# Kernel optimization log

Measured on AMD Instinct MI355X. Metric: run time of the kernel, lower is better.

## Reference

```python
import jax, jax.numpy as jnp
import numpy as np

B, S, D, H = 2, 2048, 1024, 16
DK = D // H
NEG = -1e9


def setup_inputs() -> dict:
    key = jax.random.key(0)
    ks = jax.random.split(key, 12)
    inp = {
        "query": jax.random.normal(ks[0], (B, S, D), jnp.float32),
        "key": jax.random.normal(ks[1], (B, S, D), jnp.float32),
        "value": jax.random.normal(ks[2], (B, S, D), jnp.float32),
        "mask": jax.random.randint(ks[3], (B, S), 0, 2, jnp.int32),
    }
    # 4 linears (q, k, v, out), each d_model x d_model with bias.
    scale = 1.0 / np.sqrt(D)
    for i, name in enumerate(["wq", "wk", "wv", "wo"]):
        inp[name] = jax.random.uniform(ks[4 + i], (D, D), jnp.float32, -scale, scale)
        inp["b" + name[1]] = jax.random.uniform(ks[8 + i], (D,), jnp.float32, -scale, scale)
    return inp


def _split_heads(x):  # [B,S,D] -> [B,H,S,DK]
    return x.reshape(B, S, H, DK).transpose(0, 2, 1, 3)


def reference(query, key, value, mask, wq, bq, wk, bk, wv, bv, wo, bo):
    q = _split_heads(query @ wq.T + bq)
    k = _split_heads(key @ wk.T + bk)
    v = _split_heads(value @ wv.T + bv)
    scores = jnp.einsum("bhqd,bhkd->bhqk", q, k) / jnp.sqrt(jnp.float32(DK))
    # mask: [B,S] -> [B,1,1,S]; masked_fill where mask == 0
    m = mask[:, None, None, :]
    scores = jnp.where(m == 0, NEG, scores)
    attn = jax.nn.softmax(scores, axis=-1)  # dropout p=0 (eval) -> identity
    x = jnp.einsum("bhqk,bhkd->bhqd", attn, v)
    x = x.transpose(0, 2, 1, 3).reshape(B, S, D)
    return x @ wo.T + bo
```

## Files before the change

### kernel.cpp

```cpp
#include <hip/hip_runtime.h>


typedef _Float16 f16;
typedef _Float16 f16x8 __attribute__((ext_vector_type(8)));
typedef _Float16 f16x4 __attribute__((ext_vector_type(4)));
typedef __fp16 fp16x2r __attribute__((ext_vector_type(2)));
typedef float f32x4 __attribute__((ext_vector_type(4)));

union F16x4u { f16x4 v; fp16x2r h[2]; };

#define MFMA_F16(a, b, c) __builtin_amdgcn_mfma_f32_16x16x32_f16((a), (b), (c), 0, 0, 0)
#define MFMA16(a, b, c) __builtin_amdgcn_mfma_f32_16x16x16f16((a), (b), (c), 0, 0, 0)
#define L2E 1.44269504088896340736f

__device__ __forceinline__ void gld16(const void* g, void* l) {
    __builtin_amdgcn_global_load_lds(
        (__attribute__((address_space(1))) void*)(g),
        (__attribute__((address_space(3))) void*)(l), 16, 0, 0);
}

__global__ __launch_bounds__(256) void cvt_kernel(
    const float* __restrict__ q, const float* __restrict__ k,
    const float* __restrict__ v,
    const float* __restrict__ wq, const float* __restrict__ wk,
    const float* __restrict__ wv, const float* __restrict__ wo,
    f16* __restrict__ oq, f16* __restrict__ ok, f16* __restrict__ ov,
    f16* __restrict__ owq, f16* __restrict__ owk, f16* __restrict__ owv,
    f16* __restrict__ owo)
{
    const int z = blockIdx.y;
    const float* src;
    f16* dst;
    int n;
    switch (z) {
        case 0: src = q;  dst = oq;  n = 4194304; break;
        case 1: src = k;  dst = ok;  n = 4194304; break;
        case 2: src = v;  dst = ov;  n = 4194304; break;
        case 3: src = wq; dst = owq; n = 1048576; break;
        case 4: src = wk; dst = owk; n = 1048576; break;
        case 5: src = wv; dst = owv; n = 1048576; break;
        default: src = wo; dst = owo; n = 1048576; break;
    }
    int idx = (blockIdx.x * 256 + threadIdx.x) * 8;
    if (idx >= n) return;
    float4 a = *(const float4*)(src + idx);
    float4 b = *(const float4*)(src + idx + 4);
    f16x8 h = { (f16)a.x, (f16)a.y, (f16)a.z, (f16)a.w,
                (f16)b.x, (f16)b.y, (f16)b.z, (f16)b.w };
    *(f16x8*)(dst + idx) = h;
}

__global__ __launch_bounds__(256) void proj_qkv_kernel(
    const f16* __restrict__ xq, const f16* __restrict__ xk,
    const f16* __restrict__ xv,
    const f16* __restrict__ wqh, const f16* __restrict__ wkh,
    const f16* __restrict__ wvh,
    const float* __restrict__ bq, const float* __restrict__ bk,
    const float* __restrict__ bv,
    f16* __restrict__ qh, f16* __restrict__ kh, f16* __restrict__ vt)
{
    const int z = blockIdx.z;
    const f16* X = (z == 0) ? xq : (z == 1) ? xk : xv;
    const f16* W = (z == 0) ? wqh : (z == 1) ? wkh : wvh;
    const float* bias = (z == 0) ? bq : (z == 1) ? bk : bv;
    const f16* P0 = (z < 2) ? W : X;
    const f16* P1 = (z < 2) ? X : W;

    __shared__ __align__(16) f16 smem[16384];
    f16* As = smem;
    f16* Bs = smem + 8192;
    f16* L  = smem;

    const int t = threadIdx.x;
    const int wave = t >> 6, lane = t & 63, quad = lane >> 4, l15 = lane & 15;
    const int m_base = (wave >> 1) * 64, n_base = (wave & 1) * 64;
    const int blockM = (z < 2) ? blockIdx.y * 128 : blockIdx.x * 128;
    const int blockN = (z < 2) ? blockIdx.x * 128 : blockIdx.y * 128;

    const int srow = lane >> 3;
    const int sblk = (lane & 7) ^ srow;

    f32x4 acc[4][4];
#pragma unroll
    for (int mt = 0; mt < 4; mt++)
#pragma unroll
        for (int nt = 0; nt < 4; nt++)
            acc[mt][nt] = (f32x4){0.f, 0.f, 0.f, 0.f};

    for (int k0 = 0; k0 < 1024; k0 += 64) {
        __syncthreads();
#pragma unroll
        for (int j = 0; j < 4; j++) {
            int r0 = wave * 32 + j * 8;
            gld16(&P0[(size_t)(blockM + r0 + srow) * 1024 + k0 + sblk * 8],
                  &As[r0 * 64]);
            gld16(&P1[(size_t)(blockN + r0 + srow) * 1024 + k0 + sblk * 8],
                  &Bs[r0 * 64]);
        }
        __syncthreads();

#pragma unroll
        for (int c = 0; c < 2; c++) {
            f16x8 af[4], bf[4];
#pragma unroll
            for (int mt = 0; mt < 4; mt++)
                af[mt] = *(const f16x8*)(&As[(m_base + mt * 16 + l15) * 64 +
                                             (((c * 4 + quad) ^ (l15 & 7)) << 3)]);
#pragma unroll
            for (int nt = 0; nt < 4; nt++)
                bf[nt] = *(const f16x8*)(&Bs[(n_base + nt * 16 + l15) * 64 +
                                             (((c * 4 + quad) ^ (l15 & 7)) << 3)]);
#pragma unroll
            for (int mt = 0; mt < 4; mt++)
#pragma unroll
                for (int nt = 0; nt < 4; nt++)
                    acc[mt][nt] = MFMA_F16(af[mt], bf[nt], acc[mt][nt]);
        }
    }

    if (z < 2) {
        f16* o = (z == 0) ? qh : kh;
        const float scale = (z == 0) ? 0.125f * L2E : 1.0f;
        float4 b4[4];
#pragma unroll
        for (int mt = 0; mt < 4; mt++)
            b4[mt] = *(const float4*)(&bias[blockM + m_base + mt * 16 + quad * 4]);

#pragma unroll
        for (int half = 0; half < 2; half++) {
            __syncthreads();
            if ((wave & 1) == half) {
#pragma unroll
                for (int mt = 0; mt < 4; mt++)
#pragma unroll
                    for (int nt = 0; nt < 4; nt++) {
                        f16x4 pk = {
                            (f16)((acc[mt][nt][0] + b4[mt].x) * scale),
                            (f16)((acc[mt][nt][1] + b4[mt].y) * scale),
                            (f16)((acc[mt][nt][2] + b4[mt].z) * scale),
                            (f16)((acc[mt][nt][3] + b4[mt].w) * scale) };
                        *(f16x4*)(&L[(nt * 16 + l15) * 136 +
                                     m_base + mt * 16 + quad * 4]) = pk;
                    }
            }
            __syncthreads();
#pragma unroll
            for (int pass = 0; pass < 4; pass++) {
                int unit = pass * 32 + (t >> 3);
                int hh = unit >> 6, s_loc = unit & 63;
                f16x8 vv = *(const f16x8*)(&L[s_loc * 136 + hh * 64 + (t & 7) * 8]);
                int s_glob = blockN + half * 64 + s_loc;
                int b = s_glob >> 11, s = s_glob & 2047;
                int h_glob = (blockM >> 6) + hh;
                *(f16x8*)(&o[(((size_t)(b * 16 + h_glob) * 2048 + s) << 6) +
                             (t & 7) * 8]) = vv;
            }
        }
    } else {
        float bv_[4];
#pragma unroll
        for (int nt = 0; nt < 4; nt++)
            bv_[nt] = bias[blockN + n_base + nt * 16 + l15];

#pragma unroll
        for (int half = 0; half < 2; half++) {
            __syncthreads();
            if ((wave & 1) == half) {
#pragma unroll
                for (int mt = 0; mt < 4; mt++)
#pragma unroll
                    for (int nt = 0; nt < 4; nt++) {
                        f16x4 pk = { (f16)(acc[mt][nt][0] + bv_[nt]),
                                     (f16)(acc[mt][nt][1] + bv_[nt]),
                                     (f16)(acc[mt][nt][2] + bv_[nt]),
                                     (f16)(acc[mt][nt][3] + bv_[nt]) };
                        *(f16x4*)(&L[(nt * 16 + l15) * 136 +
                                     m_base + mt * 16 + quad * 4]) = pk;
                    }
            }
            __syncthreads();
#pragma unroll
            for (int pass = 0; pass < 4; pass++) {
                int f_loc = pass * 16 + (t >> 4);
                f16x8 vv = *(const f16x8*)(&L[f_loc * 136 + (t & 15) * 8]);
                int feat = blockN + half * 64 + f_loc;
                int hh = feat >> 6, dk = feat & 63;
                int b = blockM >> 11;
                int s0 = (blockM & 2047) + (t & 15) * 8;
                *(f16x8*)(&vt[((size_t)((b * 16 + hh) * 64 + dk) << 11) + s0]) = vv;
            }
        }
    }
}

__device__ __forceinline__ void flash_stage(
    const f16* kbase, const f16* vbase, int key0,
    f16* Kb, f16* Vb, int wave, int srow8, int sblk)
{
#pragma unroll
    for (int p = 0; p < 2; p++) {
        int r0 = p * 32 + wave * 8;
        int row = r0 + srow8;
        gld16(&kbase[(size_t)(key0 + row) * 64 + sblk * 8], &Kb[r0 * 64]);
        gld16(&vbase[(size_t)row * 2048 + key0 + sblk * 8], &Vb[r0 * 64]);
    }
}

__device__ __forceinline__ void flash_phase(
    const f16* Kbuf, const f16* Vbuf, const float* bias_all, int key0,
    const f16x8 (&qf)[2][2], int quad, int l15,
    f32x4 (&O)[2][4], f32x4 (&lacc)[2])
{
    f32x4 sc[2][4];
#pragma unroll
    for (int nt = 0; nt < 4; nt++) {
        const f16* krow = &Kbuf[(nt * 16 + l15) * 64];
        f16x8 kf0 = *(const f16x8*)(&krow[(quad ^ (l15 & 7)) << 3]);
        f16x8 kf1 = *(const f16x8*)(&krow[((quad + 4) ^ (l15 & 7)) << 3]);
        float4 b4 = *(const float4*)(&bias_all[key0 + nt * 16 + quad * 4]);
#pragma unroll
        for (int cb = 0; cb < 2; cb++) {
            f32x4 z4 = (f32x4){b4.x, b4.y, b4.z, b4.w};
            z4 = MFMA_F16(kf0, qf[cb][0], z4);
            sc[cb][nt] = MFMA_F16(kf1, qf[cb][1], z4);
        }
    }
    const f16x4 ones = {(f16)1.f, (f16)1.f, (f16)1.f, (f16)1.f};
    f16x4 pf[2][4];
#pragma unroll
    for (int cb = 0; cb < 2; cb++)
#pragma unroll
        for (int nt = 0; nt < 4; nt++) {
            float p0 = exp2f(sc[cb][nt][0]);
            float p1 = exp2f(sc[cb][nt][1]);
            float p2 = exp2f(sc[cb][nt][2]);
            float p3 = exp2f(sc[cb][nt][3]);
            F16x4u u;
            u.h[0] = __builtin_amdgcn_cvt_pkrtz(p0, p1);
            u.h[1] = __builtin_amdgcn_cvt_pkrtz(p2, p3);
            pf[cb][nt] = u.v;
            lacc[cb] = MFMA16(ones, pf[cb][nt], lacc[cb]);
        }
#pragma unroll
    for (int nto = 0; nto < 4; nto++) {
        const f16* vrow = &Vbuf[(nto * 16 + l15) * 64];
#pragma unroll
        for (int nt = 0; nt < 4; nt++) {
            f16x4 vf = *(const f16x4*)(&vrow[
                (((nt * 2 + (quad >> 1)) ^ (l15 & 7)) << 3) + (quad & 1) * 4]);
            O[0][nto] = MFMA16(vf, pf[0][nt], O[0][nto]);
            O[1][nto] = MFMA16(vf, pf[1][nt], O[1][nto]);
        }
    }
}

__global__ __launch_bounds__(256) void flash_kernel(
    const f16* __restrict__ qh, const f16* __restrict__ kh,
    const f16* __restrict__ vt, const int* __restrict__ mask,
    f16* __restrict__ ctx)
{
    __shared__ __align__(16) f16 Ks0[64 * 64];
    __shared__ __align__(16) f16 Ks1[64 * 64];
    __shared__ __align__(16) f16 Vts0[64 * 64];
    __shared__ __align__(16) f16 Vts1[64 * 64];
    __shared__ float bias_all[2048];

    const int t = threadIdx.x;
    const int wave = t >> 6, lane = t & 63, quad = lane >> 4, l15 = lane & 15;
    const int bh = blockIdx.x;
    const int b = bh >> 4, h = bh & 15;
    const int q0 = blockIdx.y * 128;

    const f16* qbase = qh + (size_t)bh * (2048 * 64);
    const f16* kbase = kh + (size_t)bh * (2048 * 64);
    const f16* vbase = vt + (size_t)bh * (64 * 2048);

#pragma unroll
    for (int j = 0; j < 8; j++) {
        int i = j * 256 + t;
        bias_all[i] = (mask[b * 2048 + i] == 0) ? -1.0e9f : 0.0f;
    }

    f16x8 qf[2][2];
#pragma unroll
    for (int cb = 0; cb < 2; cb++) {
        int qrow = q0 + wave * 32 + cb * 16 + l15;
        qf[cb][0] = *(const f16x8*)(&qbase[qrow * 64 + quad * 8]);
        qf[cb][1] = *(const f16x8*)(&qbase[qrow * 64 + 32 + quad * 8]);
    }

    f32x4 O[2][4];
#pragma unroll
    for (int cb = 0; cb < 2; cb++)
#pragma unroll
        for (int n = 0; n < 4; n++) O[cb][n] = (f32x4){0.f, 0.f, 0.f, 0.f};
    f32x4 lacc[2] = {(f32x4){0.f, 0.f, 0.f, 0.f}, (f32x4){0.f, 0.f, 0.f, 0.f}};

    const int srow8 = lane >> 3;
    const int sblk = (lane & 7) ^ srow8;

    flash_stage(kbase, vbase, 0, Ks0, Vts0, wave, srow8, sblk);

    for (int k2 = 0; k2 < 16; k2++) {
        const int key0 = k2 * 128;
        __syncthreads();
        flash_stage(kbase, vbase, key0 + 64, Ks1, Vts1, wave, srow8, sblk);
        flash_phase(Ks0, Vts0, bias_all, key0, qf, quad, l15, O, lacc);
        __syncthreads();
        if (k2 < 15)
            flash_stage(kbase, vbase, key0 + 128, Ks0, Vts0, wave, srow8, sblk);
        flash_phase(Ks1, Vts1, bias_all, key0 + 64, qf, quad, l15, O, lacc);
    }

#pragma unroll
    for (int cb = 0; cb < 2; cb++) {
        const float inv_l = 1.0f / lacc[cb][0];
        int qrow = q0 + wave * 32 + cb * 16 + l15;
#pragma unroll
        for (int nto = 0; nto < 4; nto++) {
            f16x4 pk = { (f16)(O[cb][nto][0] * inv_l),
                         (f16)(O[cb][nto][1] * inv_l),
                         (f16)(O[cb][nto][2] * inv_l),
                         (f16)(O[cb][nto][3] * inv_l) };
            *(f16x4*)(&ctx[(size_t)(b * 2048 + qrow) * 1024 + h * 64 +
                           nto * 16 + quad * 4]) = pk;
        }
    }
}

__global__ __launch_bounds__(256) void proj_out_kernel(
    const f16* __restrict__ ctx, const f16* __restrict__ woh,
    const float* __restrict__ bo, float* __restrict__ out)
{
    __shared__ __align__(16) f16 As[2][128 * 64];
    __shared__ __align__(16) f16 Bs[2][64 * 64];

    const int t = threadIdx.x;
    const int wave = t >> 6, lane = t & 63, quad = lane >> 4, l15 = lane & 15;
    const int m_base = (wave >> 1) * 64, n_base = (wave & 1) * 32;
    const int blockM = blockIdx.x * 128;
    const int blockN = blockIdx.y * 64;

    const int srow = lane >> 3;
    const int sblk = (lane & 7) ^ srow;

    f32x4 acc[4][2];
#pragma unroll
    for (int mt = 0; mt < 4; mt++)
#pragma unroll
        for (int nt = 0; nt < 2; nt++)
            acc[mt][nt] = (f32x4){0.f, 0.f, 0.f, 0.f};

#pragma unroll
    for (int j = 0; j < 4; j++) {
        int r0 = wave * 32 + j * 8;
        gld16(&ctx[(size_t)(blockM + r0 + srow) * 1024 + sblk * 8],
              &As[0][r0 * 64]);
    }
#pragma unroll
    for (int j = 0; j < 2; j++) {
        int r0 = wave * 16 + j * 8;
        gld16(&woh[(size_t)(blockN + r0 + srow) * 1024 + sblk * 8],
              &Bs[0][r0 * 64]);
    }

    for (int ki = 0; ki < 16; ki++) {
        const int cur = ki & 1;
        __syncthreads();

        if (ki < 15) {
            const int k0n = (ki + 1) * 64;
#pragma unroll
            for (int j = 0; j < 4; j++) {
                int r0 = wave * 32 + j * 8;
                gld16(&ctx[(size_t)(blockM + r0 + srow) * 1024 + k0n + sblk * 8],
                      &As[cur ^ 1][r0 * 64]);
            }
#pragma unroll
            for (int j = 0; j < 2; j++) {
                int r0 = wave * 16 + j * 8;
                gld16(&woh[(size_t)(blockN + r0 + srow) * 1024 + k0n + sblk * 8],
                      &Bs[cur ^ 1][r0 * 64]);
            }
        }

#pragma unroll
        for (int c = 0; c < 2; c++) {
            f16x8 af[4], bf[2];
#pragma unroll
            for (int mt = 0; mt < 4; mt++)
                af[mt] = *(const f16x8*)(&As[cur][(m_base + mt * 16 + l15) * 64 +
                                              (((c * 4 + quad) ^ (l15 & 7)) << 3)]);
#pragma unroll
            for (int nt = 0; nt < 2; nt++)
                bf[nt] = *(const f16x8*)(&Bs[cur][(n_base + nt * 16 + l15) * 64 +
                                              (((c * 4 + quad) ^ (l15 & 7)) << 3)]);
#pragma unroll
            for (int mt = 0; mt < 4; mt++)
#pragma unroll
                for (int nt = 0; nt < 2; nt++)
                    acc[mt][nt] = MFMA_F16(af[mt], bf[nt], acc[mt][nt]);
        }
    }

    float bo_[2];
#pragma unroll
    for (int nt = 0; nt < 2; nt++)
        bo_[nt] = bo[blockN + n_base + nt * 16 + l15];

#pragma unroll
    for (int mt = 0; mt < 4; mt++) {
        int row0 = blockM + m_base + mt * 16 + quad * 4;
#pragma unroll
        for (int nt = 0; nt < 2; nt++) {
            int col_g = blockN + n_base + nt * 16 + l15;
#pragma unroll
            for (int i = 0; i < 4; i++)
                out[(size_t)(row0 + i) * 1024 + col_g] = acc[mt][nt][i] + bo_[nt];
        }
    }
}

extern "C" void kernel_launch(void* const* d_in, const int* in_sizes, int n_in,
                              void* d_out, int out_size, void* d_ws, size_t ws_size,
                              hipStream_t stream) {
    const float* query = (const float*)d_in[0];
    const float* key_  = (const float*)d_in[1];
    const float* value = (const float*)d_in[2];
    const int*   mask  = (const int*)d_in[3];
    const float* wq = (const float*)d_in[4];
    const float* bq = (const float*)d_in[5];
    const float* wk = (const float*)d_in[6];
    const float* bk = (const float*)d_in[7];
    const float* wv = (const float*)d_in[8];
    const float* bv = (const float*)d_in[9];
    const float* wo = (const float*)d_in[10];
    const float* bo = (const float*)d_in[11];
    float* out = (float*)d_out;

    f16* xq  = (f16*)d_ws;
    f16* xk  = xq  + 4194304;
    f16* xv  = xk  + 4194304;
    f16* wqh = xv  + 4194304;
    f16* wkh = wqh + 1048576;
    f16* wvh = wkh + 1048576;
    f16* woh = wvh + 1048576;
    f16* qh  = woh + 1048576;
    f16* kh  = qh  + 4194304;
    f16* vt  = kh  + 4194304;
    f16* ctx = xq;

    cvt_kernel<<<dim3(2048, 7), 256, 0, stream>>>(
        query, key_, value, wq, wk, wv, wo, xq, xk, xv, wqh, wkh, wvh, woh);
    proj_qkv_kernel<<<dim3(32, 8, 3), 256, 0, stream>>>(
        xq, xk, xv, wqh, wkh, wvh, bq, bk, bv, qh, kh, vt);
    flash_kernel<<<dim3(32, 16), 256, 0, stream>>>(qh, kh, vt, mask, ctx);
    proj_out_kernel<<<dim3(32, 16), 256, 0, stream>>>(ctx, woh, bo, out);
}
```

Baseline: 236.2 us.

## Switch flash attention inner loop to 32x32x16 MFMA with permlane swap

The flash attention phase now uses 32x32x16 f16 MFMA tiles in place of the 16x16x32 and 16x16x16 instructions. The QK^T accumulator is converted to the PV operand layout in registers with permlane32 swaps. The row-sum is accumulated with scalar adds and one cross-half shuffle instead of an extra ones-MFMA per tile. The aim is fewer MFMA issues and less LDS fragment traffic per key tile, at the cost of larger accumulator register footprints and a new lane-permutation step.

```diff
diff --git a/kernel.cpp b/kernel.cpp
--- a/kernel.cpp
+++ b/kernel.cpp
@@ -6,17 +6,29 @@
 typedef _Float16 f16x4 __attribute__((ext_vector_type(4)));
 typedef __fp16 fp16x2r __attribute__((ext_vector_type(2)));
 typedef float f32x4 __attribute__((ext_vector_type(4)));
-
-union F16x4u { f16x4 v; fp16x2r h[2]; };
+typedef float f32x16 __attribute__((ext_vector_type(16)));
+typedef unsigned u32x2 __attribute__((ext_vector_type(2)));
 
 #define MFMA_F16(a, b, c) __builtin_amdgcn_mfma_f32_16x16x32_f16((a), (b), (c), 0, 0, 0)
-#define MFMA16(a, b, c) __builtin_amdgcn_mfma_f32_16x16x16f16((a), (b), (c), 0, 0, 0)
+#define MFMA32(a, b, c) __builtin_amdgcn_mfma_f32_32x32x16_f16((a), (b), (c), 0, 0, 0)
 #define L2E 1.44269504088896340736f
 
 __device__ __forceinline__ void gld16(const void* g, void* l) {
     __builtin_amdgcn_global_load_lds(
         (__attribute__((address_space(1))) void*)(g),
         (__attribute__((address_space(3))) void*)(l), 16, 0, 0);
+}
+
+__device__ __forceinline__ void swap_halves(unsigned& a, unsigned& b) {
+#if __has_builtin(__builtin_amdgcn_permlane32_swap)
+    u32x2 r = __builtin_amdgcn_permlane32_swap(a, b, false, false);
+    a = r[0];
+    b = r[1];
+#else
+    unsigned pa = (unsigned)__shfl_xor((int)a, 32);
+    unsigned pb = (unsigned)__shfl_xor((int)b, 32);
+    if ((threadIdx.x & 32) == 0) { b = pa; } else { a = pb; }
+#endif
 }
 
 __global__ __launch_bounds__(256) void cvt_kernel(
@@ -208,49 +220,66 @@
 
 __device__ __forceinline__ void flash_phase(
     const f16* Kbuf, const f16* Vbuf, const float* bias_all, int key0,
-    const f16x8 (&qf)[2][2], int quad, int l15,
-    f32x4 (&O)[2][4], f32x4 (&lacc)[2])
-{
-    f32x4 sc[2][4];
-#pragma unroll
-    for (int nt = 0; nt < 4; nt++) {
-        const f16* krow = &Kbuf[(nt * 16 + l15) * 64];
-        f16x8 kf0 = *(const f16x8*)(&krow[(quad ^ (l15 & 7)) << 3]);
-        f16x8 kf1 = *(const f16x8*)(&krow[((quad + 4) ^ (l15 & 7)) << 3]);
-        float4 b4 = *(const float4*)(&bias_all[key0 + nt * 16 + quad * 4]);
-#pragma unroll
-        for (int cb = 0; cb < 2; cb++) {
-            f32x4 z4 = (f32x4){b4.x, b4.y, b4.z, b4.w};
-            z4 = MFMA_F16(kf0, qf[cb][0], z4);
-            sc[cb][nt] = MFMA_F16(kf1, qf[cb][1], z4);
-        }
-    }
-    const f16x4 ones = {(f16)1.f, (f16)1.f, (f16)1.f, (f16)1.f};
-    f16x4 pf[2][4];
-#pragma unroll
-    for (int cb = 0; cb < 2; cb++)
-#pragma unroll
-        for (int nt = 0; nt < 4; nt++) {
-            float p0 = exp2f(sc[cb][nt][0]);
-            float p1 = exp2f(sc[cb][nt][1]);
-            float p2 = exp2f(sc[cb][nt][2]);
-            float p3 = exp2f(sc[cb][nt][3]);
-            F16x4u u;
-            u.h[0] = __builtin_amdgcn_cvt_pkrtz(p0, p1);
-            u.h[1] = __builtin_amdgcn_cvt_pkrtz(p2, p3);
-            pf[cb][nt] = u.v;
-            lacc[cb] = MFMA16(ones, pf[cb][nt], lacc[cb]);
-        }
-#pragma unroll
-    for (int nto = 0; nto < 4; nto++) {
-        const f16* vrow = &Vbuf[(nto * 16 + l15) * 64];
-#pragma unroll
-        for (int nt = 0; nt < 4; nt++) {
-            f16x4 vf = *(const f16x4*)(&vrow[
-                (((nt * 2 + (quad >> 1)) ^ (l15 & 7)) << 3) + (quad & 1) * 4]);
-            O[0][nto] = MFMA16(vf, pf[0][nt], O[0][nto]);
-            O[1][nto] = MFMA16(vf, pf[1][nt], O[1][nto]);
-        }
+    const f16x8 (&qf)[4], int l31, int hi, int hb, int l7,
+    f32x16& O0, f32x16& O1, float& rs)
+{
+    f32x16 S[2];
+#pragma unroll
+    for (int mb = 0; mb < 2; mb++) {
+        const float* bp = &bias_all[key0 + mb * 32 + hb];
+        float4 b0 = *(const float4*)(bp);
+        float4 b1 = *(const float4*)(bp + 8);
+        float4 b2 = *(const float4*)(bp + 16);
+        float4 b3 = *(const float4*)(bp + 24);
+        S[mb] = (f32x16){b0.x, b0.y, b0.z, b0.w, b1.x, b1.y, b1.z, b1.w,
+                         b2.x, b2.y, b2.z, b2.w, b3.x, b3.y, b3.z, b3.w};
+    }
+#pragma unroll
+    for (int kc = 0; kc < 4; kc++) {
+        int pb = ((kc * 2 + hi) ^ l7) << 3;
+        f16x8 kf0 = *(const f16x8*)(&Kbuf[l31 * 64 + pb]);
+        f16x8 kf1 = *(const f16x8*)(&Kbuf[(32 + l31) * 64 + pb]);
+        S[0] = MFMA32(kf0, qf[kc], S[0]);
+        S[1] = MFMA32(kf1, qf[kc], S[1]);
+    }
+
+    f16x8 Bf[4];
+#pragma unroll
+    for (int mb = 0; mb < 2; mb++) {
+        unsigned w[8];
+        float ls = 0.f;
+#pragma unroll
+        for (int g = 0; g < 4; g++) {
+            float p0 = exp2f(S[mb][4 * g + 0]);
+            float p1 = exp2f(S[mb][4 * g + 1]);
+            float p2 = exp2f(S[mb][4 * g + 2]);
+            float p3 = exp2f(S[mb][4 * g + 3]);
+            ls += (p0 + p1) + (p2 + p3);
+            union { fp16x2r h; unsigned u; } c0, c1;
+            c0.h = __builtin_amdgcn_cvt_pkrtz(p0, p1);
+            c1.h = __builtin_amdgcn_cvt_pkrtz(p2, p3);
+            w[2 * g] = c0.u;
+            w[2 * g + 1] = c1.u;
+        }
+        rs += ls;
+        swap_halves(w[0], w[2]);
+        swap_halves(w[1], w[3]);
+        swap_halves(w[4], w[6]);
+        swap_halves(w[5], w[7]);
+        union { f16x8 v; unsigned q[4]; } bb0, bb1;
+        bb0.q[0] = w[0]; bb0.q[1] = w[1]; bb0.q[2] = w[2]; bb0.q[3] = w[3];
+        bb1.q[0] = w[4]; bb1.q[1] = w[5]; bb1.q[2] = w[6]; bb1.q[3] = w[7];
+        Bf[2 * mb] = bb0.v;
+        Bf[2 * mb + 1] = bb1.v;
+    }
+
+#pragma unroll
+    for (int kc = 0; kc < 4; kc++) {
+        int pb = ((kc * 2 + hi) ^ l7) << 3;
+        f16x8 vf0 = *(const f16x8*)(&Vbuf[l31 * 64 + pb]);
+        f16x8 vf1 = *(const f16x8*)(&Vbuf[(32 + l31) * 64 + pb]);
+        O0 = MFMA32(vf0, Bf[kc], O0);
+        O1 = MFMA32(vf1, Bf[kc], O1);
     }
 }
 
@@ -266,7 +295,8 @@
     __shared__ float bias_all[2048];
 
     const int t = threadIdx.x;
-    const int wave = t >> 6, lane = t & 63, quad = lane >> 4, l15 = lane & 15;
+    const int wave = t >> 6, lane = t & 63;
+    const int l31 = lane & 31, hi = lane >> 5, hb = hi * 4, l7 = l31 & 7;
     const int bh = blockIdx.x;
     const int b = bh >> 4, h = bh & 15;
     const int q0 = blockIdx.y * 128;
@@ -281,20 +311,14 @@
         bias_all[i] = (mask[b * 2048 + i] == 0) ? -1.0e9f : 0.0f;
     }
 
-    f16x8 qf[2][2];
-#pragma unroll
-    for (int cb = 0; cb < 2; cb++) {
-        int qrow = q0 + wave * 32 + cb * 16 + l15;
-        qf[cb][0] = *(const f16x8*)(&qbase[qrow * 64 + quad * 8]);
-        qf[cb][1] = *(const f16x8*)(&qbase[qrow * 64 + 32 + quad * 8]);
-    }
-
-    f32x4 O[2][4];
-#pragma unroll
-    for (int cb = 0; cb < 2; cb++)
-#pragma unroll
-        for (int n = 0; n < 4; n++) O[cb][n] = (f32x4){0.f, 0.f, 0.f, 0.f};
-    f32x4 lacc[2] = {(f32x4){0.f, 0.f, 0.f, 0.f}, (f32x4){0.f, 0.f, 0.f, 0.f}};
+    const int qrow = q0 + wave * 32 + l31;
+    f16x8 qf[4];
+#pragma unroll
+    for (int kc = 0; kc < 4; kc++)
+        qf[kc] = *(const f16x8*)(&qbase[(size_t)qrow * 64 + kc * 16 + hi * 8]);
+
+    f32x16 O0{}, O1{};
+    float rs = 0.f;
 
     const int srow8 = lane >> 3;
     const int sblk = (lane & 7) ^ srow8;
@@ -305,26 +329,25 @@
         const int key0 = k2 * 128;
         __syncthreads();
         flash_stage(kbase, vbase, key0 + 64, Ks1, Vts1, wave, srow8, sblk);
-        flash_phase(Ks0, Vts0, bias_all, key0, qf, quad, l15, O, lacc);
+        flash_phase(Ks0, Vts0, bias_all, key0, qf, l31, hi, hb, l7, O0, O1, rs);
         __syncthreads();
         if (k2 < 15)
             flash_stage(kbase, vbase, key0 + 128, Ks0, Vts0, wave, srow8, sblk);
-        flash_phase(Ks1, Vts1, bias_all, key0 + 64, qf, quad, l15, O, lacc);
-    }
-
-#pragma unroll
-    for (int cb = 0; cb < 2; cb++) {
-        const float inv_l = 1.0f / lacc[cb][0];
-        int qrow = q0 + wave * 32 + cb * 16 + l15;
-#pragma unroll
-        for (int nto = 0; nto < 4; nto++) {
-            f16x4 pk = { (f16)(O[cb][nto][0] * inv_l),
-                         (f16)(O[cb][nto][1] * inv_l),
-                         (f16)(O[cb][nto][2] * inv_l),
-                         (f16)(O[cb][nto][3] * inv_l) };
-            *(f16x4*)(&ctx[(size_t)(b * 2048 + qrow) * 1024 + h * 64 +
-                           nto * 16 + quad * 4]) = pk;
-        }
+        flash_phase(Ks1, Vts1, bias_all, key0 + 64, qf, l31, hi, hb, l7, O0, O1, rs);
+    }
+
+    const float l = rs + __shfl_xor(rs, 32);
+    const float inv_l = 1.0f / l;
+
+    f16* cb = &ctx[(size_t)(b * 2048 + qrow) * 1024 + h * 64];
+#pragma unroll
+    for (int g = 0; g < 4; g++) {
+        f16x4 pk0 = { (f16)(O0[4 * g + 0] * inv_l), (f16)(O0[4 * g + 1] * inv_l),
+                      (f16)(O0[4 * g + 2] * inv_l), (f16)(O0[4 * g + 3] * inv_l) };
+        f16x4 pk1 = { (f16)(O1[4 * g + 0] * inv_l), (f16)(O1[4 * g + 1] * inv_l),
+                      (f16)(O1[4 * g + 2] * inv_l), (f16)(O1[4 * g + 3] * inv_l) };
+        *(f16x4*)(&cb[8 * g + hb]) = pk0;
+        *(f16x4*)(&cb[32 + 8 * g + hb]) = pk1;
     }
 }
 
```

Measured after the change: 237.1 us. Within noise of the previous version (+0.3%).
